# Performance work log

Measured on AMD Instinct MI355X. Metric: run time of the kernel, lower is better.

## Reference

```python
import jax, jax.numpy as jnp
import numpy as np

LN2 = float(np.log(2.0))
EPS = 1e-5

def layer_norm(x, scale, bias):
    mu = jnp.mean(x, axis=-1, keepdims=True)
    var = jnp.var(x, axis=-1, keepdims=True)
    return (x - mu) * jax.lax.rsqrt(var + EPS) * scale + bias

def shifted_softplus(x):
    return jax.nn.softplus(x) - LN2

def setup_inputs() -> dict:
    key = jax.random.key(0)
    N, E, H = 50000, 800000, 128
    ks = jax.random.split(key, 12)
    s = 0.05
    inp = {
        'h_V': jax.random.normal(ks[0], (N, H), jnp.float32),
        'h_E': jax.random.normal(ks[1], (E, H), jnp.float32),
        'edge_index': jax.random.randint(ks[2], (2, E), 0, N, jnp.int64),
        # attention weights (stored [in, out])
        'W_Q': jax.random.normal(ks[3], (H, H), jnp.float32) * s,
        'W_K': jax.random.normal(ks[4], (2 * H, H), jnp.float32) * s,
        'W_V': jax.random.normal(ks[5], (2 * H, H), jnp.float32) * s,
        'W_O': jax.random.normal(ks[6], (H, H), jnp.float32) * s,
        # layernorms
        'ln1_scale': jnp.ones((H,), jnp.float32),
        'ln1_bias': jnp.zeros((H,), jnp.float32),
        'ln2_scale': jnp.ones((H,), jnp.float32),
        'ln2_bias': jnp.zeros((H,), jnp.float32),
        # FFN (num_ff == num_hidden in TransformerLayer)
        'W_in': jax.random.normal(ks[7], (H, H), jnp.float32) * s,
        'b_in': jnp.zeros((H,), jnp.float32),
        'W_out': jax.random.normal(ks[8], (H, H), jnp.float32) * s,
        'b_out': jnp.zeros((H,), jnp.float32),
    }
    return inp

def reference(h_V, h_E, edge_index, W_Q, W_K, W_V, W_O,
              ln1_scale, ln1_bias, ln2_scale, ln2_bias,
              W_in, b_in, W_out, b_out):
    N, H = h_V.shape
    E = h_E.shape[0]
    n_heads = 4
    d = H // n_heads
    row, col = edge_index[0], edge_index[1]

    # --- attention block ---
    y = layer_norm(h_V, ln1_scale, ln1_bias)
    hv_col = y[col]                                  # [E, H] gather
    he = jnp.concatenate([h_E, hv_col], axis=-1)     # [E, 2H]
    Q = (y @ W_Q).reshape(N, n_heads, d)             # [N, h, d]
    K = (he @ W_K).reshape(E, n_heads, d)            # [E, h, d]
    V = (he @ W_V).reshape(E, n_heads, d)            # [E, h, d]
    logits = jnp.sum(Q[row] * K, axis=-1)            # [E, h]

    # scatter softmax over destination node `row`
    m = jax.ops.segment_max(logits, row, num_segments=N)      # [N, h]
    m = jnp.where(jnp.isfinite(m), m, 0.0)
    ex = jnp.exp(logits - m[row])                              # [E, h]
    denom = jax.ops.segment_sum(ex, row, num_segments=N)      # [N, h]
    alpha = ex / denom[row] / jnp.sqrt(jnp.float32(d))         # faithful: scale AFTER softmax

    msg = alpha[..., None] * V                                 # [E, h, d]
    aggr = jax.ops.segment_sum(msg, row, num_segments=N)      # [N, h, d]
    attn_out = shifted_softplus(aggr.reshape(N, H)) @ W_O      # [N, H]

    h_V = h_V + attn_out  # dropout is identity (eval)

    # --- FFN block ---
    y = layer_norm(h_V, ln2_scale, ln2_bias)
    y = jax.nn.relu(y @ W_in + b_in) @ W_out + b_out
    h_V = h_V + y
    return h_V
```

## Files before the change

### kernel.cpp

```cpp
#include <hip/hip_runtime.h>


typedef __bf16 bf16x8 __attribute__((ext_vector_type(8)));
typedef float f32x4 __attribute__((ext_vector_type(4)));
typedef unsigned short u16x8 __attribute__((ext_vector_type(8)));

#define DEV static __device__ __forceinline__
#define ET 64

DEV unsigned short f2b(float f){
  union { float f; unsigned u; } v; v.f = f;
  unsigned r = (v.u + 0x7FFFu + ((v.u >> 16) & 1u)) >> 16;
  return (unsigned short)r;
}
DEV float b2f(unsigned short h){
  union { unsigned u; float f; } v; v.u = ((unsigned)h) << 16; return v.f;
}
DEV f32x4 mfma16(bf16x8 a, bf16x8 b, f32x4 c){
  return __builtin_amdgcn_mfma_f32_16x16x32_bf16(a, b, c, 0, 0, 0);
}
DEV u16x8 pack8(float4 a, float4 b){
  u16x8 p;
  p[0]=f2b(a.x); p[1]=f2b(a.y); p[2]=f2b(a.z); p[3]=f2b(a.w);
  p[4]=f2b(b.x); p[5]=f2b(b.y); p[6]=f2b(b.z); p[7]=f2b(b.w);
  return p;
}
DEV float sspf(float x){
  return fmaxf(x, 0.f) + log1pf(expf(-fabsf(x))) - 0.69314718055994531f;
}
DEV int idx64probe(const int* __restrict__ ei){
  return (ei[1] | ei[3] | ei[5] | ei[7] | ei[9]) == 0;
}
DEV int ld_row(const int* __restrict__ ei, long eg, long E, int is64, int N){
  int v = is64 ? ei[2*eg] : ei[eg];
  return min(max(v, 0), N - 1);
}
DEV int ld_col(const int* __restrict__ ei, long eg, long E, int is64, int N){
  int v = is64 ? ei[2*(E + eg)] : ei[E + eg];
  return min(max(v, 0), N - 1);
}
DEV unsigned swz(unsigned byteoff, unsigned row){
  return byteoff ^ ((row & 7u) << 4);
}
DEV void bar_lds(){
  __builtin_amdgcn_sched_barrier(0);
  asm volatile("s_waitcnt lgkmcnt(0)" ::: "memory");
  __builtin_amdgcn_s_barrier();
  __builtin_amdgcn_sched_barrier(0);
}

DEV void mma128(const unsigned short* At, const unsigned short* __restrict__ WT,
                int t, f32x4 (&acc)[4][4]){
  const int l = t & 63;
  const int wm = (t >> 7) & 1, wn = (t >> 6) & 1;
#pragma unroll
  for (int m = 0; m < 4; ++m)
#pragma unroll
    for (int n = 0; n < 4; ++n)
      acc[m][n] = f32x4{0.f, 0.f, 0.f, 0.f};
#pragma unroll
  for (int kk = 0; kk < 4; ++kk){
    bf16x8 a[4], b[4];
#pragma unroll
    for (int m = 0; m < 4; ++m){
      int row = wm*64 + m*16 + (l & 15);
      a[m] = *(const bf16x8*)((const char*)At +
              swz((unsigned)(row*256 + kk*64 + ((l >> 4) & 3)*16), (unsigned)row));
    }
#pragma unroll
    for (int n = 0; n < 4; ++n){
      int col = wn*64 + n*16 + (l & 15);
      b[n] = *(const bf16x8*)(WT + col*128 + kk*32 + ((l >> 4) & 3)*8);
    }
#pragma unroll
    for (int m = 0; m < 4; ++m)
#pragma unroll
      for (int n = 0; n < 4; ++n)
        acc[m][n] = mfma16(a[m], b[n], acc[m][n]);
  }
}

DEV void mma64(const unsigned short* Ab, const unsigned short* __restrict__ WT,
               int t, f32x4 (&acc)[2][4]){
  const int l = t & 63, wid = t >> 6, wm = wid >> 1, wn = wid & 1;
#pragma unroll
  for (int m = 0; m < 2; ++m)
#pragma unroll
    for (int n = 0; n < 4; ++n) acc[m][n] = f32x4{0.f, 0.f, 0.f, 0.f};
#pragma unroll
  for (int kk = 0; kk < 4; ++kk){
    bf16x8 a[2], b[4];
#pragma unroll
    for (int m = 0; m < 2; ++m){
      int row = wm*32 + m*16 + (l & 15);
      a[m] = *(const bf16x8*)((const char*)Ab +
          swz((unsigned)(row*256 + kk*64 + ((l >> 4) & 3)*16), (unsigned)row));
    }
#pragma unroll
    for (int n = 0; n < 4; ++n){
      int col = wn*64 + n*16 + (l & 15);
      b[n] = *(const bf16x8*)(WT + col*128 + kk*32 + ((l >> 4) & 3)*8);
    }
#pragma unroll
    for (int m = 0; m < 2; ++m)
#pragma unroll
      for (int n = 0; n < 4; ++n)
        acc[m][n] = mfma16(a[m], b[n], acc[m][n]);
  }
}
DEV void store_acc64(unsigned short* Kt, const f32x4 (&acc)[2][4], int t){
  const int l = t & 63, wid = t >> 6, wm = wid >> 1, wn = wid & 1;
#pragma unroll
  for (int m = 0; m < 2; ++m)
#pragma unroll
    for (int n = 0; n < 4; ++n)
#pragma unroll
      for (int reg = 0; reg < 4; ++reg){
        int er = wm*32 + m*16 + ((l >> 4) & 3)*4 + reg;
        int col = wn*64 + n*16 + (l & 15);
        *(unsigned short*)((char*)Kt + swz((unsigned)(er*256 + col*2), (unsigned)er))
            = f2b(acc[m][n][reg]);
      }
}

__global__ void k_zero(float4* __restrict__ p, long n){
  long i = (long)blockIdx.x * blockDim.x + threadIdx.x;
  const long st = (long)gridDim.x * blockDim.x;
  const float4 z = {0.f, 0.f, 0.f, 0.f};
  for (; i < n; i += st) p[i] = z;
}

__global__ void k_wprep(const float* __restrict__ WQ, const float* __restrict__ WK,
                        const float* __restrict__ WV, const float* __restrict__ WO,
                        const float* __restrict__ Wi, const float* __restrict__ Wo2,
                        unsigned short* WQT, unsigned short* WKtT, unsigned short* WKbT,
                        unsigned short* WVtT, unsigned short* WVbT, unsigned short* WOT,
                        unsigned short* WinT, unsigned short* WouT){
  int id = blockIdx.x * 256 + threadIdx.x;
  int n = id >> 7, k = id & 127;
  int d = n * 128 + k;
  WQT[d]  = f2b(WQ[k*128 + n]);
  WKtT[d] = f2b(WK[k*128 + n]);
  WKbT[d] = f2b(WK[(k+128)*128 + n]);
  WVtT[d] = f2b(WV[k*128 + n]);
  WVbT[d] = f2b(WV[(k+128)*128 + n]);
  WOT[d]  = f2b(WO[k*128 + n]);
  WinT[d] = f2b(Wi[k*128 + n]);
  WouT[d] = f2b(Wo2[k*128 + n]);
}

__global__ void k_hist(const int* __restrict__ ei, int* __restrict__ cnt, long E, int N){
  const int is64 = idx64probe(ei);
  long i = (long)blockIdx.x * blockDim.x + threadIdx.x;
  const long st = (long)gridDim.x * blockDim.x;
  for (; i < E; i += st) atomicAdd(&cnt[ld_row(ei, i, E, is64, N)], 1);
}

DEV int wave_incl_scan(int v, int lane){
#pragma unroll
  for (int ofs = 1; ofs < 64; ofs <<= 1){
    int u = __shfl_up(v, ofs, 64);
    if (lane >= ofs) v += u;
  }
  return v;
}

__global__ __launch_bounds__(1024) void k_scan(const int* __restrict__ cnt,
                                               int* __restrict__ cursor,
                                               int4* __restrict__ edata,
                                               long E, int N){
  __shared__ int wsum[16], woff[16];
  const int t = threadIdx.x, lane = t & 63, w = t >> 6;
  const int C = (N + 1023) / 1024;
  const int base = t * C;
  int s = 0;
  for (int j = 0; j < C; ++j) if (base + j < N) s += cnt[base + j];
  int incl = wave_incl_scan(s, lane);
  if (lane == 63) wsum[w] = incl;
  __syncthreads();
  if (t == 0){
    int run = 0;
#pragma unroll
    for (int i = 0; i < 16; ++i){ woff[i] = run; run += wsum[i]; }
  }
  __syncthreads();
  int run = woff[w] + incl - s;
  for (int j = 0; j < C; ++j)
    if (base + j < N){ cursor[base + j] = run; run += cnt[base + j]; }
  if (t < 67){
    long gi = (t == 0) ? 0 : (E + t);
    edata[gi] = make_int4(0, -2, 0, 0);
  }
}

__global__ void k_scatter(const int* __restrict__ ei, int* __restrict__ cursor,
                          int4* __restrict__ edata, long E, int N){
  const int is64 = idx64probe(ei);
  long i = (long)blockIdx.x * blockDim.x + threadIdx.x;
  const long st = (long)gridDim.x * blockDim.x;
  for (; i < E; i += st){
    int r = ld_row(ei, i, E, is64, N);
    int c = ld_col(ei, i, E, is64, N);
    int pos = atomicAdd(&cursor[r], 1);
    edata[1 + (long)pos] = make_int4((int)i, r, c, 0);
  }
}

__global__ __launch_bounds__(256) void k_nodeprep(
    const float* __restrict__ hV, const float* __restrict__ l1s, const float* __restrict__ l1b,
    const unsigned short* __restrict__ WQT, const unsigned short* __restrict__ WKbT,
    const unsigned short* __restrict__ WVbT,
    unsigned short* __restrict__ Qbf, unsigned short* __restrict__ YKVbf, int N){
  __shared__ unsigned short At[128*128];
  __shared__ float ps[256], pss[256];
  __shared__ float scs[128], bis[128];
  const int t = threadIdx.x;
  if (t < 128){ scs[t] = l1s[t]; bis[t] = l1b[t]; }
  const int r0 = blockIdx.x * 128;
  const int rl = t & 127, hf = t >> 7;
  const int r = r0 + rl;
  const float4* xp = (const float4*)(hV + (size_t)r*128 + hf*64);
  float s = 0.f, ss = 0.f;
  if (r < N){
#pragma unroll
    for (int i = 0; i < 16; ++i){
      float4 v = xp[i];
      s  += (v.x + v.y) + (v.z + v.w);
      ss += (v.x*v.x + v.y*v.y) + (v.z*v.z + v.w*v.w);
    }
  }
  ps[t] = s; pss[t] = ss;
  __syncthreads();
  const float mu  = (ps[t] + ps[t ^ 128]) * 0.0078125f;
  const float var = (pss[t] + pss[t ^ 128]) * 0.0078125f - mu*mu;
  const float rs  = rsqrtf(var + 1e-5f);
#pragma unroll
  for (int i = 0; i < 8; ++i){
    const int c = hf*64 + i*8;
    u16x8 p = {0,0,0,0,0,0,0,0};
    if (r < N){
      float4 v0 = xp[2*i], v1 = xp[2*i+1];
      p[0] = f2b((v0.x - mu)*rs*scs[c+0] + bis[c+0]);
      p[1] = f2b((v0.y - mu)*rs*scs[c+1] + bis[c+1]);
      p[2] = f2b((v0.z - mu)*rs*scs[c+2] + bis[c+2]);
      p[3] = f2b((v0.w - mu)*rs*scs[c+3] + bis[c+3]);
      p[4] = f2b((v1.x - mu)*rs*scs[c+4] + bis[c+4]);
      p[5] = f2b((v1.y - mu)*rs*scs[c+5] + bis[c+5]);
      p[6] = f2b((v1.z - mu)*rs*scs[c+6] + bis[c+6]);
      p[7] = f2b((v1.w - mu)*rs*scs[c+7] + bis[c+7]);
    }
    *(u16x8*)((char*)At + swz((unsigned)(rl*256 + c*2), (unsigned)rl)) = p;
  }
  __syncthreads();
  const int l = t & 63, wm = (t >> 7) & 1, wn = (t >> 6) & 1;
  f32x4 acc[4][4];
  for (int g = 0; g < 3; ++g){
    const unsigned short* WT = (g == 0) ? WQT : (g == 1) ? WKbT : WVbT;
    mma128(At, WT, t, acc);
#pragma unroll
    for (int m = 0; m < 4; ++m)
#pragma unroll
      for (int reg = 0; reg < 4; ++reg){
        int row = wm*64 + m*16 + ((l >> 4) & 3)*4 + reg;
        int gr = r0 + row;
        if (gr < N){
#pragma unroll
          for (int n = 0; n < 4; ++n){
            int col = wn*64 + n*16 + (l & 15);
            unsigned short v = f2b(acc[m][n][reg]);
            if (g == 0)      Qbf[(size_t)gr*128 + col] = v;
            else if (g == 1) YKVbf[(size_t)gr*256 + col] = v;
            else             YKVbf[(size_t)gr*256 + 128 + col] = v;
          }
        }
      }
  }
}

__global__ __launch_bounds__(256, 3) void k_edge(
    const float* __restrict__ hE,
    const unsigned short* __restrict__ WKtT, const unsigned short* __restrict__ WVtT,
    const unsigned short* __restrict__ Qbf, const unsigned short* __restrict__ YKVbf,
    const int4* __restrict__ edata,
    float* __restrict__ num, float* __restrict__ den,
    long E, long NT){
  __shared__ unsigned short Ab[ET*128];
  __shared__ unsigned short Kt[ET*128];
  __shared__ float aS[ET][4];
  __shared__ int rowsT[2][ET + 2];
  __shared__ int colT[2][ET];

  const int t = threadIdx.x;
  const int rr = t & 63, sl = t >> 6;
  const long b0 = blockIdx.x, G = gridDim.x;
  const long ntloc = (b0 < NT) ? ((NT - 1 - b0) / G + 1) : 0;
  if (ntloc == 0) return;

  auto tileof = [&](long i) -> long {
    long tt = b0 + i * G; return (tt < NT) ? tt : (NT - 1);
  };

  int4 edc = edata[1 + tileof(0)*ET + rr];
  long pe0 = (long)edc.x; pe0 = pe0 < 0 ? 0 : pe0;
  const float4* hp0 = (const float4*)(hE + (size_t)pe0*128 + sl*32);
  float4 h0=hp0[0], h1=hp0[1], h2=hp0[2], h3=hp0[3],
         h4=hp0[4], h5=hp0[5], h6=hp0[6], h7=hp0[7];
  int4 edn = edata[1 + tileof(1)*ET + rr];

  for (long it = 0; it < ntloc; ++it){
    const int par = (int)(it & 1);
    if (t < ET){ rowsT[par][1 + t] = edc.y; colT[par][t] = edc.z; }
    if (t == 64) rowsT[par][0]      = edata[tileof(it)*ET].y;
    if (t == 65) rowsT[par][ET + 1] = edata[1 + tileof(it)*ET + ET].y;
    {
      unsigned base = (unsigned)(rr*256 + sl*64);
      unsigned x = ((unsigned)(rr & 7)) << 4;
      *(u16x8*)((char*)Ab + ((base     ) ^ x)) = pack8(h0, h1);
      *(u16x8*)((char*)Ab + ((base + 16) ^ x)) = pack8(h2, h3);
      *(u16x8*)((char*)Ab + ((base + 32) ^ x)) = pack8(h4, h5);
      *(u16x8*)((char*)Ab + ((base + 48) ^ x)) = pack8(h6, h7);
    }
    edc = edn;
    edn = edata[1 + tileof(it + 2)*ET + rr];
    {
      long pe = (long)edc.x; pe = pe < 0 ? 0 : pe;
      const float4* np = (const float4*)(hE + (size_t)pe*128 + sl*32);
      h0 = np[0]; h1 = np[1]; h2 = np[2]; h3 = np[3];
      h4 = np[4]; h5 = np[5]; h6 = np[6]; h7 = np[7];
    }
    bar_lds();
    { f32x4 acc[2][4]; mma64(Ab, WKtT, t, acc); store_acc64(Kt, acc, t); }
    bar_lds();
    {
      const int e = t >> 2, q = t & 3;
      const int r = rowsT[par][1 + e], c = colT[par][e];
      const int ra = max(r, 0), ca = max(c, 0);
      const u16x8* qp = (const u16x8*)(Qbf  + (size_t)ra*128 + q*32);
      const u16x8* kp = (const u16x8*)(YKVbf + (size_t)ca*256 + q*32);
      const unsigned xb = ((unsigned)(e & 7)) << 4;
      float pl = 0.f;
#pragma unroll
      for (int k = 0; k < 4; ++k){
        u16x8 qv = qp[k], yk = kp[k];
        u16x8 kv = *(const u16x8*)((const char*)Kt +
            (((unsigned)(e*256 + q*64 + k*16)) ^ xb));
#pragma unroll
        for (int j = 0; j < 8; ++j) pl += b2f(qv[j]) * (b2f(kv[j]) + b2f(yk[j]));
      }
      aS[e][q] = (r >= 0) ? expf(pl) : 0.f;
    }
    bar_lds();
    { f32x4 acc[2][4]; mma64(Ab, WVtT, t, acc); store_acc64(Kt, acc, t); }
    bar_lds();
    {
      const int e = t >> 2, q = t & 3;
      const int ca = max(colT[par][e], 0);
      const u16x8* vp = (const u16x8*)(YKVbf + (size_t)ca*256 + 128 + q*32);
      const unsigned xb = ((unsigned)(e & 7)) << 4;
#pragma unroll
      for (int k = 0; k < 4; ++k){
        u16x8* pp = (u16x8*)((char*)Kt + (((unsigned)(e*256 + q*64 + k*16)) ^ xb));
        u16x8 a = *pp, b = vp[k], o;
#pragma unroll
        for (int j = 0; j < 8; ++j) o[j] = f2b(b2f(a[j]) + b2f(b[j]));
        *pp = o;
      }
    }
    bar_lds();
    {
      const int c = t & 127, half = t >> 7, hh = c >> 5;
      const int eb = half * 32;
      float accv = 0.f, accd = 0.f;
      int cur = rowsT[par][1 + eb], rs = eb;
      for (int e = eb; e < eb + 32; ++e){
        int r = rowsT[par][1 + e];
        if (r != cur){
          if (cur >= 0){
            bool own = (rowsT[par][rs] != cur);
            float* np = num + (size_t)cur*128 + c;
            if (own) *np = accv; else atomicAdd(np, accv);
            if (c < 4){
              float* dp = den + (size_t)cur*4 + c;
              if (own) *dp = accd; else atomicAdd(dp, accd);
            }
          }
          cur = r; rs = e; accv = 0.f; accd = 0.f;
        }
        float a = aS[e][hh];
        accv += a * b2f(*(const unsigned short*)((const char*)Kt +
                  swz((unsigned)(e*256 + c*2), (unsigned)e)));
        if (c < 4) accd += aS[e][c];
      }
      if (cur >= 0){
        bool own = (rowsT[par][rs] != cur) && (rowsT[par][1 + eb + 32] != cur);
        float* np = num + (size_t)cur*128 + c;
        if (own) *np = accv; else atomicAdd(np, accv);
        if (c < 4){
          float* dp = den + (size_t)cur*4 + c;
          if (own) *dp = accd; else atomicAdd(dp, accd);
        }
      }
    }
  }
}

__global__ __launch_bounds__(256, 2) void k_post(
    const float* __restrict__ hV, const float* __restrict__ num,
    const float* __restrict__ den,
    const unsigned short* __restrict__ WOT, const unsigned short* __restrict__ WinT,
    const unsigned short* __restrict__ WouT,
    const float* __restrict__ l2s, const float* __restrict__ l2b,
    const float* __restrict__ bin, const float* __restrict__ bou,
    float* __restrict__ out, int N){
  __shared__ unsigned short At[128*128];
  __shared__ float ps[128][2], pq[128][2];
  __shared__ float scs[128], bis[128], binS[128], bouS[128];
  const int t = threadIdx.x;
  if (t < 128){ scs[t] = l2s[t]; bis[t] = l2b[t]; binS[t] = bin[t]; bouS[t] = bou[t]; }
  const int r0 = blockIdx.x * 128;
  const int rl = t & 127, hf = t >> 7;
  const int r = r0 + rl;
  const float inv = 0.17677669529663687f;
  float i0 = 0.f, i1 = 0.f;
  if (r < N){
    float d0 = den[(size_t)r*4 + 2*hf], d1 = den[(size_t)r*4 + 2*hf + 1];
    i0 = (d0 > 0.f) ? inv / d0 : 0.f;
    i1 = (d1 > 0.f) ? inv / d1 : 0.f;
  }
  const float4* ap = (const float4*)(num + (size_t)r*128 + hf*64);
#pragma unroll
  for (int i = 0; i < 8; ++i){
    u16x8 p = {0,0,0,0,0,0,0,0};
    if (r < N){
      float sc = (i < 4) ? i0 : i1;
      float4 v0 = ap[2*i], v1 = ap[2*i+1];
      p[0]=f2b(sspf(v0.x*sc)); p[1]=f2b(sspf(v0.y*sc)); p[2]=f2b(sspf(v0.z*sc)); p[3]=f2b(sspf(v0.w*sc));
      p[4]=f2b(sspf(v1.x*sc)); p[5]=f2b(sspf(v1.y*sc)); p[6]=f2b(sspf(v1.z*sc)); p[7]=f2b(sspf(v1.w*sc));
    }
    *(u16x8*)((char*)At + swz((unsigned)(rl*256 + hf*128 + i*16), (unsigned)rl)) = p;
  }
  __syncthreads();
  const int l = t & 63, wm = (t >> 7) & 1, wn = (t >> 6) & 1;
  f32x4 acc[4][4];
  mma128(At, WOT, t, acc);
  float h1[4][4][4];
#pragma unroll
  for (int m = 0; m < 4; ++m)
#pragma unroll
    for (int reg = 0; reg < 4; ++reg){
      int er = wm*64 + m*16 + ((l >> 4) & 3)*4 + reg;
      int gr = r0 + er;
#pragma unroll
      for (int n = 0; n < 4; ++n){
        int col = wn*64 + n*16 + (l & 15);
        h1[m][n][reg] = acc[m][n][reg] + ((gr < N) ? hV[(size_t)gr*128 + col] : 0.f);
      }
    }
#pragma unroll
  for (int m = 0; m < 4; ++m)
#pragma unroll
    for (int reg = 0; reg < 4; ++reg){
      float s = 0.f, q = 0.f;
#pragma unroll
      for (int n = 0; n < 4; ++n){ float v = h1[m][n][reg]; s += v; q += v*v; }
#pragma unroll
      for (int o = 1; o < 16; o <<= 1){ s += __shfl_xor(s, o); q += __shfl_xor(q, o); }
      if ((l & 15) == 0){
        int er = wm*64 + m*16 + ((l >> 4) & 3)*4 + reg;
        ps[er][wn] = s; pq[er][wn] = q;
      }
    }
  __syncthreads();
#pragma unroll
  for (int m = 0; m < 4; ++m)
#pragma unroll
    for (int reg = 0; reg < 4; ++reg){
      int er = wm*64 + m*16 + ((l >> 4) & 3)*4 + reg;
      float mu  = (ps[er][0] + ps[er][1]) * 0.0078125f;
      float var = (pq[er][0] + pq[er][1]) * 0.0078125f - mu*mu;
      float rsv = rsqrtf(var + 1e-5f);
#pragma unroll
      for (int n = 0; n < 4; ++n){
        int col = wn*64 + n*16 + (l & 15);
        float yv = (h1[m][n][reg] - mu)*rsv*scs[col] + bis[col];
        *(unsigned short*)((char*)At + swz((unsigned)(er*256 + col*2), (unsigned)er)) = f2b(yv);
      }
    }
  __syncthreads();
  mma128(At, WinT, t, acc);
  __syncthreads();
#pragma unroll
  for (int m = 0; m < 4; ++m)
#pragma unroll
    for (int reg = 0; reg < 4; ++reg){
      int er = wm*64 + m*16 + ((l >> 4) & 3)*4 + reg;
#pragma unroll
      for (int n = 0; n < 4; ++n){
        int col = wn*64 + n*16 + (l & 15);
        float v = acc[m][n][reg] + binS[col];
        *(unsigned short*)((char*)At + swz((unsigned)(er*256 + col*2), (unsigned)er))
            = f2b(fmaxf(v, 0.f));
      }
    }
  __syncthreads();
  mma128(At, WouT, t, acc);
#pragma unroll
  for (int m = 0; m < 4; ++m)
#pragma unroll
    for (int reg = 0; reg < 4; ++reg){
      int er = wm*64 + m*16 + ((l >> 4) & 3)*4 + reg;
      int gr = r0 + er;
      if (gr < N){
#pragma unroll
        for (int n = 0; n < 4; ++n){
          int col = wn*64 + n*16 + (l & 15);
          out[(size_t)gr*128 + col] = acc[m][n][reg] + bouS[col] + h1[m][n][reg];
        }
      }
    }
}

extern "C" void kernel_launch(void* const* d_in, const int* in_sizes, int n_in,
                              void* d_out, int out_size, void* d_ws, size_t ws_size,
                              hipStream_t stream)
{
  const float* hV  = (const float*)d_in[0];
  const float* hE  = (const float*)d_in[1];
  const int*   ei  = (const int*)d_in[2];
  const float* WQ  = (const float*)d_in[3];
  const float* WK  = (const float*)d_in[4];
  const float* WV  = (const float*)d_in[5];
  const float* WO  = (const float*)d_in[6];
  const float* l1s = (const float*)d_in[7];
  const float* l1b = (const float*)d_in[8];
  const float* l2s = (const float*)d_in[9];
  const float* l2b = (const float*)d_in[10];
  const float* Wi  = (const float*)d_in[11];
  const float* bi  = (const float*)d_in[12];
  const float* Wo2 = (const float*)d_in[13];
  const float* bo  = (const float*)d_in[14];
  float* out = (float*)d_out;

  const int  N = in_sizes[0] / 128;
  const long E = (long)in_sizes[1] / 128;
  const long NT = (E + ET - 1) / ET;

  char* ws = (char*)d_ws;
  size_t off = 0;
  auto alloc = [&](size_t b){ size_t o = off; off += (b + 255) & ~(size_t)255; return o; };
  const size_t WB = 128*128*sizeof(unsigned short);
  size_t oWQT = alloc(WB), oWKtT = alloc(WB), oWKbT = alloc(WB);
  size_t oWVtT = alloc(WB), oWVbT = alloc(WB), oWOT = alloc(WB);
  size_t oWinT = alloc(WB), oWouT = alloc(WB);
  size_t oQ    = alloc((size_t)N*128*2);
  size_t oYKV  = alloc((size_t)N*256*2);
  size_t oED   = alloc((size_t)(E + 70)*16);
  size_t oCUR  = alloc((size_t)N*4);
  size_t oCNT  = alloc((size_t)N*4);
  size_t oDEN  = alloc((size_t)N*4*4);
  size_t oNUM  = alloc((size_t)N*128*4);
  size_t zero_bytes = (oNUM + (size_t)N*128*4) - oCNT;

  unsigned short* WQT  = (unsigned short*)(ws + oWQT);
  unsigned short* WKtT = (unsigned short*)(ws + oWKtT);
  unsigned short* WKbT = (unsigned short*)(ws + oWKbT);
  unsigned short* WVtT = (unsigned short*)(ws + oWVtT);
  unsigned short* WVbT = (unsigned short*)(ws + oWVbT);
  unsigned short* WOT  = (unsigned short*)(ws + oWOT);
  unsigned short* WinT = (unsigned short*)(ws + oWinT);
  unsigned short* WouT = (unsigned short*)(ws + oWouT);
  unsigned short* Qbf  = (unsigned short*)(ws + oQ);
  unsigned short* YKVbf= (unsigned short*)(ws + oYKV);
  int4* edata  = (int4*)(ws + oED);
  int* cursor  = (int*)(ws + oCUR);
  int* cnt     = (int*)(ws + oCNT);
  float* den   = (float*)(ws + oDEN);
  float* num   = (float*)(ws + oNUM);

  const int nbN = (N + 127) / 128;
  const int nbe = (int)((E + 255) / 256);
  const int gE  = (int)((NT < 768) ? NT : 768);

  k_zero<<<2048, 256, 0, stream>>>((float4*)(ws + oCNT), (long)(zero_bytes / 16));
  k_wprep<<<64, 256, 0, stream>>>(WQ, WK, WV, WO, Wi, Wo2,
                                  WQT, WKtT, WKbT, WVtT, WVbT, WOT, WinT, WouT);
  k_nodeprep<<<nbN, 256, 0, stream>>>(hV, l1s, l1b, WQT, WKbT, WVbT, Qbf, YKVbf, N);
  k_hist<<<nbe, 256, 0, stream>>>(ei, cnt, E, N);
  k_scan<<<1, 1024, 0, stream>>>(cnt, cursor, edata, E, N);
  k_scatter<<<nbe, 256, 0, stream>>>(ei, cursor, edata, E, N);
  k_edge<<<gE, 256, 0, stream>>>(hE, WKtT, WVtT, Qbf, YKVbf,
                                 edata, num, den, E, NT);
  k_post<<<nbN, 256, 0, stream>>>(hV, num, den, WOT, WinT, WouT,
                                  l2s, l2b, bi, bo, out, N);
}
```

Measured before the change: 917.4 us.

## Pre-permute edge features into sorted bf16 buffer for streaming edge kernel

Result: slower. 1.024 ms (+11.6%).

```diff
diff --git a/kernel.cpp b/kernel.cpp
--- a/kernel.cpp
+++ b/kernel.cpp
@@ -168,7 +168,8 @@
 __global__ __launch_bounds__(1024) void k_scan(const int* __restrict__ cnt,
                                                int* __restrict__ cursor,
                                                int4* __restrict__ edata,
-                                               long E, int N){
+                                               unsigned short* hEs,
+                                               long E, long NT, int N){
   __shared__ int wsum[16], woff[16];
   const int t = threadIdx.x, lane = t & 63, w = t >> 6;
   const int C = (N + 1023) / 1024;
@@ -191,10 +192,18 @@
     long gi = (t == 0) ? 0 : (E + t);
     edata[gi] = make_int4(0, -2, 0, 0);
   }
+  if (hEs){
+    long tailB = (NT*ET - E) * 256;
+    if ((long)t * 16 < tailB){
+      u16x8 z = {0,0,0,0,0,0,0,0};
+      *(u16x8*)((char*)hEs + E*256 + (long)t*16) = z;
+    }
+  }
 }
 
 __global__ void k_scatter(const int* __restrict__ ei, int* __restrict__ cursor,
-                          int4* __restrict__ edata, long E, int N){
+                          int4* __restrict__ edata, int* __restrict__ invpos,
+                          long E, int N){
   const int is64 = idx64probe(ei);
   long i = (long)blockIdx.x * blockDim.x + threadIdx.x;
   const long st = (long)gridDim.x * blockDim.x;
@@ -203,6 +212,24 @@
     int c = ld_col(ei, i, E, is64, N);
     int pos = atomicAdd(&cursor[r], 1);
     edata[1 + (long)pos] = make_int4((int)i, r, c, 0);
+    invpos[i] = pos;
+  }
+}
+
+__global__ __launch_bounds__(256) void k_sortE(
+    const float* __restrict__ hE, const int* __restrict__ invpos,
+    unsigned short* __restrict__ hEs, long E){
+  const int s = threadIdx.x & 7;
+  const int eo = threadIdx.x >> 3;
+  const long stride = (long)gridDim.x * 32;
+  for (long e = (long)blockIdx.x * 32 + eo; e < E; e += stride){
+    const float4* src = (const float4*)(hE + e*128 + s*16);
+    float4 f0 = src[0], f1 = src[1], f2 = src[2], f3 = src[3];
+    long pos = invpos[e];
+    unsigned x = ((unsigned)(pos & 7)) << 4;
+    char* dst = (char*)hEs + pos*256;
+    *(u16x8*)(dst + (((unsigned)(s*32))      ^ x)) = pack8(f0, f1);
+    *(u16x8*)(dst + (((unsigned)(s*32 + 16)) ^ x)) = pack8(f2, f3);
   }
 }
 
@@ -277,8 +304,8 @@
   }
 }
 
-__global__ __launch_bounds__(256, 3) void k_edge(
-    const float* __restrict__ hE,
+__global__ __launch_bounds__(256, 3) void k_edge_s(
+    const unsigned short* __restrict__ hEs,
     const unsigned short* __restrict__ WKtT, const unsigned short* __restrict__ WVtT,
     const unsigned short* __restrict__ Qbf, const unsigned short* __restrict__ YKVbf,
     const int4* __restrict__ edata,
@@ -288,83 +315,103 @@
   __shared__ unsigned short Kt[ET*128];
   __shared__ float aS[ET][4];
   __shared__ int rowsT[2][ET + 2];
-  __shared__ int colT[2][ET];
 
   const int t = threadIdx.x;
-  const int rr = t & 63, sl = t >> 6;
+  const int er = t >> 2, q = t & 3;
   const long b0 = blockIdx.x, G = gridDim.x;
   const long ntloc = (b0 < NT) ? ((NT - 1 - b0) / G + 1) : 0;
   if (ntloc == 0) return;
-
   auto tileof = [&](long i) -> long {
     long tt = b0 + i * G; return (tt < NT) ? tt : (NT - 1);
   };
 
-  int4 edc = edata[1 + tileof(0)*ET + rr];
-  long pe0 = (long)edc.x; pe0 = pe0 < 0 ? 0 : pe0;
-  const float4* hp0 = (const float4*)(hE + (size_t)pe0*128 + sl*32);
-  float4 h0=hp0[0], h1=hp0[1], h2=hp0[2], h3=hp0[3],
-         h4=hp0[4], h5=hp0[5], h6=hp0[6], h7=hp0[7];
-  int4 edn = edata[1 + tileof(1)*ET + rr];
+  int4 edA = edata[1 + tileof(0)*ET + er];
+  int4 edB = edata[1 + tileof(1)*ET + er];
+  int sA0 = edata[tileof(0)*ET].y,  sA1 = edata[1 + tileof(0)*ET + ET].y;
+  int sB0 = edata[tileof(1)*ET].y,  sB1 = edata[1 + tileof(1)*ET + ET].y;
+  u16x8 g0, g1, g2, g3, yk0, yk1, yk2, yk3, yv0, yv1, yv2, yv3;
+  {
+    const char* hp = (const char*)hEs + (size_t)tileof(0)*ET*256 + er*256 + q*64;
+    g0 = *(const u16x8*)(hp);      g1 = *(const u16x8*)(hp + 16);
+    g2 = *(const u16x8*)(hp + 32); g3 = *(const u16x8*)(hp + 48);
+    const char* kp = (const char*)YKVbf + (size_t)max(edA.z, 0)*512 + q*64;
+    yk0 = *(const u16x8*)(kp);      yk1 = *(const u16x8*)(kp + 16);
+    yk2 = *(const u16x8*)(kp + 32); yk3 = *(const u16x8*)(kp + 48);
+    const char* vp = kp + 256;
+    yv0 = *(const u16x8*)(vp);      yv1 = *(const u16x8*)(vp + 16);
+    yv2 = *(const u16x8*)(vp + 32); yv3 = *(const u16x8*)(vp + 48);
+  }
 
   for (long it = 0; it < ntloc; ++it){
     const int par = (int)(it & 1);
-    if (t < ET){ rowsT[par][1 + t] = edc.y; colT[par][t] = edc.z; }
-    if (t == 64) rowsT[par][0]      = edata[tileof(it)*ET].y;
-    if (t == 65) rowsT[par][ET + 1] = edata[1 + tileof(it)*ET + ET].y;
-    {
-      unsigned base = (unsigned)(rr*256 + sl*64);
-      unsigned x = ((unsigned)(rr & 7)) << 4;
-      *(u16x8*)((char*)Ab + ((base     ) ^ x)) = pack8(h0, h1);
-      *(u16x8*)((char*)Ab + ((base + 16) ^ x)) = pack8(h2, h3);
-      *(u16x8*)((char*)Ab + ((base + 32) ^ x)) = pack8(h4, h5);
-      *(u16x8*)((char*)Ab + ((base + 48) ^ x)) = pack8(h6, h7);
-    }
-    edc = edn;
-    edn = edata[1 + tileof(it + 2)*ET + rr];
-    {
-      long pe = (long)edc.x; pe = pe < 0 ? 0 : pe;
-      const float4* np = (const float4*)(hE + (size_t)pe*128 + sl*32);
-      h0 = np[0]; h1 = np[1]; h2 = np[2]; h3 = np[3];
-      h4 = np[4]; h5 = np[5]; h6 = np[6]; h7 = np[7];
+    if (q == 0) rowsT[par][1 + er] = edA.y;
+    if (t == 0){ rowsT[par][0] = sA0; rowsT[par][1 + ET] = sA1; }
+    {
+      char* ab = (char*)Ab + er*256 + q*64;
+      *(u16x8*)(ab)      = g0; *(u16x8*)(ab + 16) = g1;
+      *(u16x8*)(ab + 32) = g2; *(u16x8*)(ab + 48) = g3;
+    }
+    edA = edB; sA0 = sB0; sA1 = sB1;
+    edB = edata[1 + tileof(it + 2)*ET + er];
+    sB0 = edata[tileof(it + 2)*ET].y;
+    sB1 = edata[1 + tileof(it + 2)*ET + ET].y;
+    {
+      const char* hp = (const char*)hEs + (size_t)tileof(it + 1)*ET*256 + er*256 + q*64;
+      g0 = *(const u16x8*)(hp);      g1 = *(const u16x8*)(hp + 16);
+      g2 = *(const u16x8*)(hp + 32); g3 = *(const u16x8*)(hp + 48);
     }
     bar_lds();
     { f32x4 acc[2][4]; mma64(Ab, WKtT, t, acc); store_acc64(Kt, acc, t); }
     bar_lds();
     {
-      const int e = t >> 2, q = t & 3;
-      const int r = rowsT[par][1 + e], c = colT[par][e];
-      const int ra = max(r, 0), ca = max(c, 0);
-      const u16x8* qp = (const u16x8*)(Qbf  + (size_t)ra*128 + q*32);
-      const u16x8* kp = (const u16x8*)(YKVbf + (size_t)ca*256 + q*32);
-      const unsigned xb = ((unsigned)(e & 7)) << 4;
+      const int r = rowsT[par][1 + er];
+      const int ra = max(r, 0);
+      const char* qp = (const char*)Qbf + (size_t)ra*256 + q*64;
+      u16x8 q0 = *(const u16x8*)(qp),      q1 = *(const u16x8*)(qp + 16),
+            q2 = *(const u16x8*)(qp + 32), q3 = *(const u16x8*)(qp + 48);
+      const unsigned xb = ((unsigned)(er & 7)) << 4;
+      const char* kb = (const char*)Kt;
+      u16x8 c0 = *(const u16x8*)(kb + (((unsigned)(er*256 + q*64))      ^ xb));
+      u16x8 c1 = *(const u16x8*)(kb + (((unsigned)(er*256 + q*64 + 16)) ^ xb));
+      u16x8 c2 = *(const u16x8*)(kb + (((unsigned)(er*256 + q*64 + 32)) ^ xb));
+      u16x8 c3 = *(const u16x8*)(kb + (((unsigned)(er*256 + q*64 + 48)) ^ xb));
       float pl = 0.f;
 #pragma unroll
-      for (int k = 0; k < 4; ++k){
-        u16x8 qv = qp[k], yk = kp[k];
-        u16x8 kv = *(const u16x8*)((const char*)Kt +
-            (((unsigned)(e*256 + q*64 + k*16)) ^ xb));
-#pragma unroll
-        for (int j = 0; j < 8; ++j) pl += b2f(qv[j]) * (b2f(kv[j]) + b2f(yk[j]));
-      }
-      aS[e][q] = (r >= 0) ? expf(pl) : 0.f;
+      for (int j = 0; j < 8; ++j){
+        pl += b2f(q0[j]) * (b2f(c0[j]) + b2f(yk0[j]));
+        pl += b2f(q1[j]) * (b2f(c1[j]) + b2f(yk1[j]));
+        pl += b2f(q2[j]) * (b2f(c2[j]) + b2f(yk2[j]));
+        pl += b2f(q3[j]) * (b2f(c3[j]) + b2f(yk3[j]));
+      }
+      aS[er][q] = (r >= 0) ? expf(pl) : 0.f;
     }
     bar_lds();
     { f32x4 acc[2][4]; mma64(Ab, WVtT, t, acc); store_acc64(Kt, acc, t); }
     bar_lds();
     {
-      const int e = t >> 2, q = t & 3;
-      const int ca = max(colT[par][e], 0);
-      const u16x8* vp = (const u16x8*)(YKVbf + (size_t)ca*256 + 128 + q*32);
-      const unsigned xb = ((unsigned)(e & 7)) << 4;
-#pragma unroll
-      for (int k = 0; k < 4; ++k){
-        u16x8* pp = (u16x8*)((char*)Kt + (((unsigned)(e*256 + q*64 + k*16)) ^ xb));
-        u16x8 a = *pp, b = vp[k], o;
-#pragma unroll
-        for (int j = 0; j < 8; ++j) o[j] = f2b(b2f(a[j]) + b2f(b[j]));
-        *pp = o;
-      }
+      const unsigned xb = ((unsigned)(er & 7)) << 4;
+      char* kb = (char*)Kt;
+      u16x8* p0 = (u16x8*)(kb + (((unsigned)(er*256 + q*64))      ^ xb));
+      u16x8* p1 = (u16x8*)(kb + (((unsigned)(er*256 + q*64 + 16)) ^ xb));
+      u16x8* p2 = (u16x8*)(kb + (((unsigned)(er*256 + q*64 + 32)) ^ xb));
+      u16x8* p3 = (u16x8*)(kb + (((unsigned)(er*256 + q*64 + 48)) ^ xb));
+      u16x8 a0 = *p0, a1 = *p1, a2 = *p2, a3 = *p3, o0, o1, o2, o3;
+#pragma unroll
+      for (int j = 0; j < 8; ++j){
+        o0[j] = f2b(b2f(a0[j]) + b2f(yv0[j]));
+        o1[j] = f2b(b2f(a1[j]) + b2f(yv1[j]));
+        o2[j] = f2b(b2f(a2[j]) + b2f(yv2[j]));
+        o3[j] = f2b(b2f(a3[j]) + b2f(yv3[j]));
+      }
+      *p0 = o0; *p1 = o1; *p2 = o2; *p3 = o3;
+    }
+    {
+      const char* kp = (const char*)YKVbf + (size_t)max(edA.z, 0)*512 + q*64;
+      yk0 = *(const u16x8*)(kp);      yk1 = *(const u16x8*)(kp + 16);
+      yk2 = *(const u16x8*)(kp + 32); yk3 = *(const u16x8*)(kp + 48);
+      const char* vp = kp + 256;
+      yv0 = *(const u16x8*)(vp);      yv1 = *(const u16x8*)(vp + 16);
+      yv2 = *(const u16x8*)(vp + 32); yv3 = *(const u16x8*)(vp + 48);
     }
     bar_lds();
     {
@@ -404,6 +451,132 @@
   }
 }
 
+__global__ __launch_bounds__(256, 3) void k_edge_g(
+    const float* __restrict__ hE,
+    const unsigned short* __restrict__ WKtT, const unsigned short* __restrict__ WVtT,
+    const unsigned short* __restrict__ Qbf, const unsigned short* __restrict__ YKVbf,
+    const int4* __restrict__ edata,
+    float* __restrict__ num, float* __restrict__ den,
+    long E, long NT){
+  __shared__ unsigned short Ab[ET*128];
+  __shared__ unsigned short Kt[ET*128];
+  __shared__ float aS[ET][4];
+  __shared__ int rowsT[2][ET + 2];
+  __shared__ int colT[2][ET];
+
+  const int t = threadIdx.x;
+  const int rr = t & 63, sl = t >> 6;
+  const long b0 = blockIdx.x, G = gridDim.x;
+  const long ntloc = (b0 < NT) ? ((NT - 1 - b0) / G + 1) : 0;
+  if (ntloc == 0) return;
+  auto tileof = [&](long i) -> long {
+    long tt = b0 + i * G; return (tt < NT) ? tt : (NT - 1);
+  };
+
+  int4 edc = edata[1 + tileof(0)*ET + rr];
+  long pe0 = (long)edc.x; pe0 = pe0 < 0 ? 0 : pe0;
+  const float4* hp0 = (const float4*)(hE + (size_t)pe0*128 + sl*32);
+  float4 h0=hp0[0], h1=hp0[1], h2=hp0[2], h3=hp0[3],
+         h4=hp0[4], h5=hp0[5], h6=hp0[6], h7=hp0[7];
+  int4 edn = edata[1 + tileof(1)*ET + rr];
+
+  for (long it = 0; it < ntloc; ++it){
+    const int par = (int)(it & 1);
+    if (t < ET){ rowsT[par][1 + t] = edc.y; colT[par][t] = edc.z; }
+    if (t == 64) rowsT[par][0]      = edata[tileof(it)*ET].y;
+    if (t == 65) rowsT[par][ET + 1] = edata[1 + tileof(it)*ET + ET].y;
+    {
+      unsigned base = (unsigned)(rr*256 + sl*64);
+      unsigned x = ((unsigned)(rr & 7)) << 4;
+      *(u16x8*)((char*)Ab + ((base     ) ^ x)) = pack8(h0, h1);
+      *(u16x8*)((char*)Ab + ((base + 16) ^ x)) = pack8(h2, h3);
+      *(u16x8*)((char*)Ab + ((base + 32) ^ x)) = pack8(h4, h5);
+      *(u16x8*)((char*)Ab + ((base + 48) ^ x)) = pack8(h6, h7);
+    }
+    edc = edn;
+    edn = edata[1 + tileof(it + 2)*ET + rr];
+    {
+      long pe = (long)edc.x; pe = pe < 0 ? 0 : pe;
+      const float4* np = (const float4*)(hE + (size_t)pe*128 + sl*32);
+      h0 = np[0]; h1 = np[1]; h2 = np[2]; h3 = np[3];
+      h4 = np[4]; h5 = np[5]; h6 = np[6]; h7 = np[7];
+    }
+    bar_lds();
+    { f32x4 acc[2][4]; mma64(Ab, WKtT, t, acc); store_acc64(Kt, acc, t); }
+    bar_lds();
+    {
+      const int e = t >> 2, q = t & 3;
+      const int r = rowsT[par][1 + e], c = colT[par][e];
+      const int ra = max(r, 0), ca = max(c, 0);
+      const u16x8* qp = (const u16x8*)(Qbf  + (size_t)ra*128 + q*32);
+      const u16x8* kp = (const u16x8*)(YKVbf + (size_t)ca*256 + q*32);
+      const unsigned xb = ((unsigned)(e & 7)) << 4;
+      float pl = 0.f;
+#pragma unroll
+      for (int k = 0; k < 4; ++k){
+        u16x8 qv = qp[k], yk = kp[k];
+        u16x8 kv = *(const u16x8*)((const char*)Kt +
+            (((unsigned)(e*256 + q*64 + k*16)) ^ xb));
+#pragma unroll
+        for (int j = 0; j < 8; ++j) pl += b2f(qv[j]) * (b2f(kv[j]) + b2f(yk[j]));
+      }
+      aS[e][q] = (r >= 0) ? expf(pl) : 0.f;
+    }
+    bar_lds();
+    { f32x4 acc[2][4]; mma64(Ab, WVtT, t, acc); store_acc64(Kt, acc, t); }
+    bar_lds();
+    {
+      const int e = t >> 2, q = t & 3;
+      const int ca = max(colT[par][e], 0);
+      const u16x8* vp = (const u16x8*)(YKVbf + (size_t)ca*256 + 128 + q*32);
+      const unsigned xb = ((unsigned)(e & 7)) << 4;
+#pragma unroll
+      for (int k = 0; k < 4; ++k){
+        u16x8* pp = (u16x8*)((char*)Kt + (((unsigned)(e*256 + q*64 + k*16)) ^ xb));
+        u16x8 a = *pp, b = vp[k], o;
+#pragma unroll
+        for (int j = 0; j < 8; ++j) o[j] = f2b(b2f(a[j]) + b2f(b[j]));
+        *pp = o;
+      }
+    }
+    bar_lds();
+    {
+      const int c = t & 127, half = t >> 7, hh = c >> 5;
+      const int eb = half * 32;
+      float accv = 0.f, accd = 0.f;
+      int cur = rowsT[par][1 + eb], rs = eb;
+      for (int e = eb; e < eb + 32; ++e){
+        int r = rowsT[par][1 + e];
+        if (r != cur){
+          if (cur >= 0){
+            bool own = (rowsT[par][rs] != cur);
+            float* np = num + (size_t)cur*128 + c;
+            if (own) *np = accv; else atomicAdd(np, accv);
+            if (c < 4){
+              float* dp = den + (size_t)cur*4 + c;
+              if (own) *dp = accd; else atomicAdd(dp, accd);
+            }
+          }
+          cur = r; rs = e; accv = 0.f; accd = 0.f;
+        }
+        float a = aS[e][hh];
+        accv += a * b2f(*(const unsigned short*)((const char*)Kt +
+                  swz((unsigned)(e*256 + c*2), (unsigned)e)));
+        if (c < 4) accd += aS[e][c];
+      }
+      if (cur >= 0){
+        bool own = (rowsT[par][rs] != cur) && (rowsT[par][1 + eb + 32] != cur);
+        float* np = num + (size_t)cur*128 + c;
+        if (own) *np = accv; else atomicAdd(np, accv);
+        if (c < 4){
+          float* dp = den + (size_t)cur*4 + c;
+          if (own) *dp = accd; else atomicAdd(dp, accd);
+        }
+      }
+    }
+  }
+}
+
 __global__ __launch_bounds__(256, 2) void k_post(
     const float* __restrict__ hV, const float* __restrict__ num,
     const float* __restrict__ den,
@@ -555,11 +728,14 @@
   size_t oQ    = alloc((size_t)N*128*2);
   size_t oYKV  = alloc((size_t)N*256*2);
   size_t oED   = alloc((size_t)(E + 70)*16);
+  size_t oINV  = alloc((size_t)E*4);
   size_t oCUR  = alloc((size_t)N*4);
   size_t oCNT  = alloc((size_t)N*4);
   size_t oDEN  = alloc((size_t)N*4*4);
   size_t oNUM  = alloc((size_t)N*128*4);
   size_t zero_bytes = (oNUM + (size_t)N*128*4) - oCNT;
+  size_t oHES  = alloc((size_t)NT*ET*256);
+  const bool streamMode = (off <= ws_size);
 
   unsigned short* WQT  = (unsigned short*)(ws + oWQT);
   unsigned short* WKtT = (unsigned short*)(ws + oWKtT);
@@ -572,10 +748,12 @@
   unsigned short* Qbf  = (unsigned short*)(ws + oQ);
   unsigned short* YKVbf= (unsigned short*)(ws + oYKV);
   int4* edata  = (int4*)(ws + oED);
-  int* cursor  = (int*)(ws + oCUR);
-  int* cnt     = (int*)(ws + oCNT);
+  int*  invpos = (int*)(ws + oINV);
+  int*  cursor = (int*)(ws + oCUR);
+  int*  cnt    = (int*)(ws + oCNT);
   float* den   = (float*)(ws + oDEN);
   float* num   = (float*)(ws + oNUM);
+  unsigned short* hEs = streamMode ? (unsigned short*)(ws + oHES) : nullptr;
 
   const int nbN = (N + 127) / 128;
   const int nbe = (int)((E + 255) / 256);
@@ -586,10 +764,16 @@
                                   WQT, WKtT, WKbT, WVtT, WVbT, WOT, WinT, WouT);
   k_nodeprep<<<nbN, 256, 0, stream>>>(hV, l1s, l1b, WQT, WKbT, WVbT, Qbf, YKVbf, N);
   k_hist<<<nbe, 256, 0, stream>>>(ei, cnt, E, N);
-  k_scan<<<1, 1024, 0, stream>>>(cnt, cursor, edata, E, N);
-  k_scatter<<<nbe, 256, 0, stream>>>(ei, cursor, edata, E, N);
-  k_edge<<<gE, 256, 0, stream>>>(hE, WKtT, WVtT, Qbf, YKVbf,
-                                 edata, num, den, E, NT);
+  k_scan<<<1, 1024, 0, stream>>>(cnt, cursor, edata, hEs, E, NT, N);
+  k_scatter<<<nbe, 256, 0, stream>>>(ei, cursor, edata, invpos, E, N);
+  if (streamMode){
+    k_sortE<<<2048, 256, 0, stream>>>(hE, invpos, hEs, E);
+    k_edge_s<<<gE, 256, 0, stream>>>(hEs, WKtT, WVtT, Qbf, YKVbf,
+                                     edata, num, den, E, NT);
+  } else {
+    k_edge_g<<<gE, 256, 0, stream>>>(hE, WKtT, WVtT, Qbf, YKVbf,
+                                     edata, num, den, E, NT);
+  }
   k_post<<<nbN, 256, 0, stream>>>(hV, num, den, WOT, WinT, WouT,
                                   l2s, l2b, bi, bo, out, N);
 }
```

## Shrink edge tile to 32 and prefetch gathered node K/V rows

Applied to the files above, without the earlier changes.

After: 1.180 ms. 28.6% more time.

```diff
diff --git a/kernel.cpp b/kernel.cpp
--- a/kernel.cpp
+++ b/kernel.cpp
@@ -6,7 +6,7 @@
 typedef unsigned short u16x8 __attribute__((ext_vector_type(8)));
 
 #define DEV static __device__ __forceinline__
-#define ET 64
+#define ET 32
 
 DEV unsigned short f2b(float f){
   union { float f; unsigned u; } v; v.f = f;
@@ -80,47 +80,35 @@
   }
 }
 
-DEV void mma64(const unsigned short* Ab, const unsigned short* __restrict__ WT,
-               int t, f32x4 (&acc)[2][4]){
+DEV void mma32(const unsigned short* Ab, const unsigned short* __restrict__ WT,
+               int t, f32x4 (&acc)[4]){
   const int l = t & 63, wid = t >> 6, wm = wid >> 1, wn = wid & 1;
 #pragma unroll
-  for (int m = 0; m < 2; ++m)
-#pragma unroll
-    for (int n = 0; n < 4; ++n) acc[m][n] = f32x4{0.f, 0.f, 0.f, 0.f};
+  for (int n = 0; n < 4; ++n) acc[n] = f32x4{0.f, 0.f, 0.f, 0.f};
 #pragma unroll
   for (int kk = 0; kk < 4; ++kk){
-    bf16x8 a[2], b[4];
-#pragma unroll
-    for (int m = 0; m < 2; ++m){
-      int row = wm*32 + m*16 + (l & 15);
-      a[m] = *(const bf16x8*)((const char*)Ab +
-          swz((unsigned)(row*256 + kk*64 + ((l >> 4) & 3)*16), (unsigned)row));
-    }
+    int row = wm*16 + (l & 15);
+    bf16x8 a = *(const bf16x8*)((const char*)Ab +
+        swz((unsigned)(row*256 + kk*64 + ((l >> 4) & 3)*16), (unsigned)row));
 #pragma unroll
     for (int n = 0; n < 4; ++n){
       int col = wn*64 + n*16 + (l & 15);
-      b[n] = *(const bf16x8*)(WT + col*128 + kk*32 + ((l >> 4) & 3)*8);
-    }
-#pragma unroll
-    for (int m = 0; m < 2; ++m)
-#pragma unroll
-      for (int n = 0; n < 4; ++n)
-        acc[m][n] = mfma16(a[m], b[n], acc[m][n]);
-  }
-}
-DEV void store_acc64(unsigned short* Kt, const f32x4 (&acc)[2][4], int t){
+      bf16x8 b = *(const bf16x8*)(WT + col*128 + kk*32 + ((l >> 4) & 3)*8);
+      acc[n] = mfma16(a, b, acc[n]);
+    }
+  }
+}
+DEV void store_acc32(unsigned short* Kt, const f32x4 (&acc)[4], int t){
   const int l = t & 63, wid = t >> 6, wm = wid >> 1, wn = wid & 1;
 #pragma unroll
-  for (int m = 0; m < 2; ++m)
-#pragma unroll
-    for (int n = 0; n < 4; ++n)
-#pragma unroll
-      for (int reg = 0; reg < 4; ++reg){
-        int er = wm*32 + m*16 + ((l >> 4) & 3)*4 + reg;
-        int col = wn*64 + n*16 + (l & 15);
-        *(unsigned short*)((char*)Kt + swz((unsigned)(er*256 + col*2), (unsigned)er))
-            = f2b(acc[m][n][reg]);
-      }
+  for (int n = 0; n < 4; ++n)
+#pragma unroll
+    for (int reg = 0; reg < 4; ++reg){
+      int er = wm*16 + ((l >> 4) & 3)*4 + reg;
+      int col = wn*64 + n*16 + (l & 15);
+      *(unsigned short*)((char*)Kt + swz((unsigned)(er*256 + col*2), (unsigned)er))
+          = f2b(acc[n][reg]);
+    }
 }
 
 __global__ void k_zero(float4* __restrict__ p, long n){
@@ -277,7 +265,7 @@
   }
 }
 
-__global__ __launch_bounds__(256, 3) void k_edge(
+__global__ __launch_bounds__(256, 5) void k_edge(
     const float* __restrict__ hE,
     const unsigned short* __restrict__ WKtT, const unsigned short* __restrict__ WVtT,
     const unsigned short* __restrict__ Qbf, const unsigned short* __restrict__ YKVbf,
@@ -288,91 +276,95 @@
   __shared__ unsigned short Kt[ET*128];
   __shared__ float aS[ET][4];
   __shared__ int rowsT[2][ET + 2];
-  __shared__ int colT[2][ET];
 
   const int t = threadIdx.x;
-  const int rr = t & 63, sl = t >> 6;
+  const int er = t >> 3, s = t & 7;
   const long b0 = blockIdx.x, G = gridDim.x;
   const long ntloc = (b0 < NT) ? ((NT - 1 - b0) / G + 1) : 0;
   if (ntloc == 0) return;
-
   auto tileof = [&](long i) -> long {
     long tt = b0 + i * G; return (tt < NT) ? tt : (NT - 1);
   };
 
-  int4 edc = edata[1 + tileof(0)*ET + rr];
-  long pe0 = (long)edc.x; pe0 = pe0 < 0 ? 0 : pe0;
-  const float4* hp0 = (const float4*)(hE + (size_t)pe0*128 + sl*32);
-  float4 h0=hp0[0], h1=hp0[1], h2=hp0[2], h3=hp0[3],
-         h4=hp0[4], h5=hp0[5], h6=hp0[6], h7=hp0[7];
-  int4 edn = edata[1 + tileof(1)*ET + rr];
+  int4 edA = edata[1 + tileof(0)*ET + er];
+  int4 edB = edata[1 + tileof(1)*ET + er];
+  int sA0 = edata[tileof(0)*ET].y,  sA1 = edata[1 + tileof(0)*ET + ET].y;
+  int sB0 = edata[tileof(1)*ET].y,  sB1 = edata[1 + tileof(1)*ET + ET].y;
+  float4 h0, h1, h2, h3;
+  u16x8 yk0, yk1, yv0, yv1;
+  {
+    long pe = (long)edA.x; pe = pe < 0 ? 0 : pe;
+    const float4* hp = (const float4*)(hE + (size_t)pe*128 + s*16);
+    h0 = hp[0]; h1 = hp[1]; h2 = hp[2]; h3 = hp[3];
+    const char* kp = (const char*)YKVbf + (size_t)max(edA.z, 0)*512 + s*32;
+    yk0 = *(const u16x8*)(kp); yk1 = *(const u16x8*)(kp + 16);
+    const char* vp = kp + 256;
+    yv0 = *(const u16x8*)(vp); yv1 = *(const u16x8*)(vp + 16);
+  }
 
   for (long it = 0; it < ntloc; ++it){
     const int par = (int)(it & 1);
-    if (t < ET){ rowsT[par][1 + t] = edc.y; colT[par][t] = edc.z; }
-    if (t == 64) rowsT[par][0]      = edata[tileof(it)*ET].y;
-    if (t == 65) rowsT[par][ET + 1] = edata[1 + tileof(it)*ET + ET].y;
+    const unsigned xb = ((unsigned)(er & 7)) << 4;
+    if (s == 0) rowsT[par][1 + er] = edA.y;
+    if (t == 0){ rowsT[par][0] = sA0; rowsT[par][ET + 1] = sA1; }
+    *(u16x8*)((char*)Ab + (((unsigned)(er*256 + s*32))      ^ xb)) = pack8(h0, h1);
+    *(u16x8*)((char*)Ab + (((unsigned)(er*256 + s*32 + 16)) ^ xb)) = pack8(h2, h3);
+    edA = edB; sA0 = sB0; sA1 = sB1;
+    edB = edata[1 + tileof(it + 2)*ET + er];
+    sB0 = edata[tileof(it + 2)*ET].y;
+    sB1 = edata[1 + tileof(it + 2)*ET + ET].y;
     {
-      unsigned base = (unsigned)(rr*256 + sl*64);
-      unsigned x = ((unsigned)(rr & 7)) << 4;
-      *(u16x8*)((char*)Ab + ((base     ) ^ x)) = pack8(h0, h1);
-      *(u16x8*)((char*)Ab + ((base + 16) ^ x)) = pack8(h2, h3);
-      *(u16x8*)((char*)Ab + ((base + 32) ^ x)) = pack8(h4, h5);
-      *(u16x8*)((char*)Ab + ((base + 48) ^ x)) = pack8(h6, h7);
-    }
-    edc = edn;
-    edn = edata[1 + tileof(it + 2)*ET + rr];
-    {
-      long pe = (long)edc.x; pe = pe < 0 ? 0 : pe;
-      const float4* np = (const float4*)(hE + (size_t)pe*128 + sl*32);
-      h0 = np[0]; h1 = np[1]; h2 = np[2]; h3 = np[3];
-      h4 = np[4]; h5 = np[5]; h6 = np[6]; h7 = np[7];
+      long pe = (long)edA.x; pe = pe < 0 ? 0 : pe;
+      const float4* hp = (const float4*)(hE + (size_t)pe*128 + s*16);
+      h0 = hp[0]; h1 = hp[1]; h2 = hp[2]; h3 = hp[3];
     }
     bar_lds();
-    { f32x4 acc[2][4]; mma64(Ab, WKtT, t, acc); store_acc64(Kt, acc, t); }
+    { f32x4 acc[4]; mma32(Ab, WKtT, t, acc); store_acc32(Kt, acc, t); }
     bar_lds();
     {
-      const int e = t >> 2, q = t & 3;
-      const int r = rowsT[par][1 + e], c = colT[par][e];
-      const int ra = max(r, 0), ca = max(c, 0);
-      const u16x8* qp = (const u16x8*)(Qbf  + (size_t)ra*128 + q*32);
-      const u16x8* kp = (const u16x8*)(YKVbf + (size_t)ca*256 + q*32);
-      const unsigned xb = ((unsigned)(e & 7)) << 4;
+      const int r = rowsT[par][1 + er];
+      const int ra = max(r, 0);
+      const char* qp = (const char*)Qbf + (size_t)ra*256 + s*32;
+      u16x8 q0 = *(const u16x8*)(qp), q1 = *(const u16x8*)(qp + 16);
+      u16x8 c0 = *(const u16x8*)((const char*)Kt + (((unsigned)(er*256 + s*32))      ^ xb));
+      u16x8 c1 = *(const u16x8*)((const char*)Kt + (((unsigned)(er*256 + s*32 + 16)) ^ xb));
       float pl = 0.f;
 #pragma unroll
-      for (int k = 0; k < 4; ++k){
-        u16x8 qv = qp[k], yk = kp[k];
-        u16x8 kv = *(const u16x8*)((const char*)Kt +
-            (((unsigned)(e*256 + q*64 + k*16)) ^ xb));
-#pragma unroll
-        for (int j = 0; j < 8; ++j) pl += b2f(qv[j]) * (b2f(kv[j]) + b2f(yk[j]));
-      }
-      aS[e][q] = (r >= 0) ? expf(pl) : 0.f;
+      for (int j = 0; j < 8; ++j){
+        pl += b2f(q0[j]) * (b2f(c0[j]) + b2f(yk0[j]));
+        pl += b2f(q1[j]) * (b2f(c1[j]) + b2f(yk1[j]));
+      }
+      float full = pl + __shfl_xor(pl, 1);
+      if (!(s & 1)) aS[er][s >> 1] = (r >= 0) ? expf(full) : 0.f;
     }
     bar_lds();
-    { f32x4 acc[2][4]; mma64(Ab, WVtT, t, acc); store_acc64(Kt, acc, t); }
+    { f32x4 acc[4]; mma32(Ab, WVtT, t, acc); store_acc32(Kt, acc, t); }
     bar_lds();
     {
-      const int e = t >> 2, q = t & 3;
-      const int ca = max(colT[par][e], 0);
-      const u16x8* vp = (const u16x8*)(YKVbf + (size_t)ca*256 + 128 + q*32);
-      const unsigned xb = ((unsigned)(e & 7)) << 4;
-#pragma unroll
-      for (int k = 0; k < 4; ++k){
-        u16x8* pp = (u16x8*)((char*)Kt + (((unsigned)(e*256 + q*64 + k*16)) ^ xb));
-        u16x8 a = *pp, b = vp[k], o;
-#pragma unroll
-        for (int j = 0; j < 8; ++j) o[j] = f2b(b2f(a[j]) + b2f(b[j]));
-        *pp = o;
-      }
+      u16x8* p0 = (u16x8*)((char*)Kt + (((unsigned)(er*256 + s*32))      ^ xb));
+      u16x8* p1 = (u16x8*)((char*)Kt + (((unsigned)(er*256 + s*32 + 16)) ^ xb));
+      u16x8 a0 = *p0, a1 = *p1, o0, o1;
+#pragma unroll
+      for (int j = 0; j < 8; ++j){
+        o0[j] = f2b(b2f(a0[j]) + b2f(yv0[j]));
+        o1[j] = f2b(b2f(a1[j]) + b2f(yv1[j]));
+      }
+      *p0 = o0; *p1 = o1;
+    }
+    {
+      const char* kp = (const char*)YKVbf + (size_t)max(edA.z, 0)*512 + s*32;
+      yk0 = *(const u16x8*)(kp); yk1 = *(const u16x8*)(kp + 16);
+      const char* vp = kp + 256;
+      yv0 = *(const u16x8*)(vp); yv1 = *(const u16x8*)(vp + 16);
     }
     bar_lds();
     {
       const int c = t & 127, half = t >> 7, hh = c >> 5;
-      const int eb = half * 32;
+      const int eb = half * 16;
       float accv = 0.f, accd = 0.f;
       int cur = rowsT[par][1 + eb], rs = eb;
-      for (int e = eb; e < eb + 32; ++e){
+#pragma unroll
+      for (int e = eb; e < eb + 16; ++e){
         int r = rowsT[par][1 + e];
         if (r != cur){
           if (cur >= 0){
@@ -392,7 +384,7 @@
         if (c < 4) accd += aS[e][c];
       }
       if (cur >= 0){
-        bool own = (rowsT[par][rs] != cur) && (rowsT[par][1 + eb + 32] != cur);
+        bool own = (rowsT[par][rs] != cur) && (rowsT[par][1 + eb + 16] != cur);
         float* np = num + (size_t)cur*128 + c;
         if (own) *np = accv; else atomicAdd(np, accv);
         if (c < 4){
@@ -572,14 +564,14 @@
   unsigned short* Qbf  = (unsigned short*)(ws + oQ);
   unsigned short* YKVbf= (unsigned short*)(ws + oYKV);
   int4* edata  = (int4*)(ws + oED);
-  int* cursor  = (int*)(ws + oCUR);
-  int* cnt     = (int*)(ws + oCNT);
+  int*  cursor = (int*)(ws + oCUR);
+  int*  cnt    = (int*)(ws + oCNT);
   float* den   = (float*)(ws + oDEN);
   float* num   = (float*)(ws + oNUM);
 
   const int nbN = (N + 127) / 128;
   const int nbe = (int)((E + 255) / 256);
-  const int gE  = (int)((NT < 768) ? NT : 768);
+  const int gE  = (int)((NT < 1280) ? NT : 1280);
 
   k_zero<<<2048, 256, 0, stream>>>((float4*)(ws + oCNT), (long)(zero_bytes / 16));
   k_wprep<<<64, 256, 0, stream>>>(WQ, WK, WV, WO, Wi, Wo2,
```
